# Kernel optimization log

Measured on AMD Instinct MI355X. Metric: run time of the kernel, lower is better.

Reference implementation:

```python
import jax, jax.numpy as jnp
import numpy as np

DECAY = 0.9  # decay_const buffer (learn_decay=False)


def setup_inputs() -> dict:
    key = jax.random.key(0)
    ks = jax.random.split(key, 6)
    B, T, D = 64, 512, 768
    spk_hist = jax.random.normal(ks[0], (B, T, D), dtype=jnp.float32)
    act_hist = jax.random.normal(ks[1], (B, T, D), dtype=jnp.float32)
    spk_mask = jax.random.randint(ks[2], (B, T), 0, 2).astype(jnp.float32)
    act_mask = jax.random.randint(ks[3], (B, T), 0, 2).astype(jnp.float32)
    spk_mean = jax.random.normal(ks[4], (B, D), dtype=jnp.float32)
    act_mean = jax.random.normal(ks[5], (B, D), dtype=jnp.float32)
    mix_logits = jnp.zeros((2,), dtype=jnp.float32)
    return {"spk_hist": spk_hist, "spk_mask": spk_mask,
            "act_hist": act_hist, "act_mask": act_mask,
            "spk_mean": spk_mean, "act_mean": act_mean,
            "mix_logits": mix_logits}


def ema_pool(X, mask, decay):
    # X: [B,T,D], mask: [B,T] (1 valid, 0 pad) -> (h [B,D], has_any [B])
    B, T, D = X.shape
    one_minus = 1.0 - decay

    def step(carry, xm):
        h, has_any = carry          # [B,D], [B,1]
        xt, mt = xm                 # [B,D], [B]
        mt = mt[:, None]            # [B,1]
        h_new = decay * h + one_minus * xt
        h = mt * h_new + (1.0 - mt) * h
        has_any = jnp.minimum(has_any + mt, 1.0)
        return (h, has_any), None

    h0 = jnp.zeros((B, D), X.dtype)
    a0 = jnp.zeros((B, 1), X.dtype)
    (h, has_any), _ = jax.lax.scan(
        step, (h0, a0), (jnp.swapaxes(X, 0, 1), mask.T))
    return h, has_any[:, 0]


def reference(spk_hist, spk_mask, act_hist, act_mask, spk_mean, act_mean, mix_logits):
    c_spk, spk_nonempty = ema_pool(spk_hist, spk_mask, DECAY)
    c_act, act_nonempty = ema_pool(act_hist, act_mask, DECAY)
    c_spk = jnp.where((spk_nonempty == 0)[:, None], spk_mean, c_spk)
    c_act = jnp.where((act_nonempty == 0)[:, None], act_mean, c_act)
    w = jax.nn.softmax(mix_logits, axis=0)
    c = w[0] * c_spk + w[1] * c_act
    return (c, c_spk, c_act, w)
```

## Files before the change

kernel.cpp:

```cpp
#include <hip/hip_runtime.h>

#define B 64
#define T 512
#define D 768
#define NSEG 8
#define TSEG 64
#define LOG2_DECAY (-0.15200309344504995f)

#define WS_P  0
#define WS_NE (2 * B * NSEG * D)

__global__ __launch_bounds__(192) void pool_kernel(
    const float* __restrict__ spk_hist, const float* __restrict__ act_hist,
    const float* __restrict__ spk_mask, const float* __restrict__ act_mask,
    float* __restrict__ ws)
{
    const int blk = blockIdx.x;
    const int seg = blk & (NSEG - 1);
    const int b   = (blk >> 3) & (B - 1);
    const int s   = blk >> 9;

    const int tid  = threadIdx.x;
    const int lane = tid & 63;
    const int wave = tid >> 6;

    __shared__ float    wsm[TSEG];
    __shared__ float    cw[TSEG];
    __shared__ int      ct[TSEG];
    __shared__ unsigned wt[2];
    __shared__ int      Mcnt;

    const float* mask = s ? act_mask : spk_mask;
    unsigned bits = 0, cnt = 0;
    if (tid < 128) {
        const float4 mv = ((const float4*)(mask + b * T))[tid];
        bits = (mv.x > 0.5f ? 1u : 0u) | (mv.y > 0.5f ? 2u : 0u) |
               (mv.z > 0.5f ? 4u : 0u) | (mv.w > 0.5f ? 8u : 0u);
        cnt = __popc(bits);
    }
    unsigned v = cnt;
    #pragma unroll
    for (int off = 1; off < 64; off <<= 1) {
        const unsigned u = __shfl_up(v, off);
        if (lane >= off) v += u;
    }
    if (wave < 2 && lane == 63) wt[wave] = v;
    __syncthreads();
    const unsigned S = wt[0] + wt[1];

    if (tid >= seg * 16 && tid < (seg + 1) * 16) {
        unsigned run = (v - cnt) + (wave == 1 ? wt[0] : 0u);
        const int lbase = (tid - seg * 16) * 4;
        #pragma unroll
        for (int j = 0; j < 4; ++j) {
            float w = 0.0f;
            if (bits & (1u << j)) {
                run += 1;
                w = 0.1f * exp2f((float)(S - run) * LOG2_DECAY);
            }
            wsm[lbase + j] = w;
        }
    }
    __syncthreads();

    if (tid < 64) {
        const float wv = wsm[tid];
        const unsigned long long bal = __ballot(wv != 0.0f);
        if (wv != 0.0f) {
            const int pos = __popcll(bal & ((1ull << tid) - 1ull));
            cw[pos] = wv;
            ct[pos] = tid;
        }
        if (tid == 0) Mcnt = __popcll(bal);
    }
    __syncthreads();

    const float* hist = s ? act_hist : spk_hist;
    const float* Xb = hist + (size_t)(b * T + seg * TSEG) * D + tid * 4;

    float4 acc = make_float4(0.f, 0.f, 0.f, 0.f);
    const int M = Mcnt;
    int k = 0;
    for (; k + 4 <= M; k += 4) {
        const int   t0 = ct[k],   t1 = ct[k+1], t2 = ct[k+2], t3 = ct[k+3];
        const float w0 = cw[k],   w1 = cw[k+1], w2 = cw[k+2], w3 = cw[k+3];
        const float4 x0 = *(const float4*)(Xb + t0 * D);
        const float4 x1 = *(const float4*)(Xb + t1 * D);
        const float4 x2 = *(const float4*)(Xb + t2 * D);
        const float4 x3 = *(const float4*)(Xb + t3 * D);
        acc.x = fmaf(w0, x0.x, acc.x); acc.y = fmaf(w0, x0.y, acc.y);
        acc.z = fmaf(w0, x0.z, acc.z); acc.w = fmaf(w0, x0.w, acc.w);
        acc.x = fmaf(w1, x1.x, acc.x); acc.y = fmaf(w1, x1.y, acc.y);
        acc.z = fmaf(w1, x1.z, acc.z); acc.w = fmaf(w1, x1.w, acc.w);
        acc.x = fmaf(w2, x2.x, acc.x); acc.y = fmaf(w2, x2.y, acc.y);
        acc.z = fmaf(w2, x2.z, acc.z); acc.w = fmaf(w2, x2.w, acc.w);
        acc.x = fmaf(w3, x3.x, acc.x); acc.y = fmaf(w3, x3.y, acc.y);
        acc.z = fmaf(w3, x3.z, acc.z); acc.w = fmaf(w3, x3.w, acc.w);
    }
    for (; k < M; ++k) {
        const float w = cw[k];
        const float4 x = *(const float4*)(Xb + ct[k] * D);
        acc.x = fmaf(w, x.x, acc.x); acc.y = fmaf(w, x.y, acc.y);
        acc.z = fmaf(w, x.z, acc.z); acc.w = fmaf(w, x.w, acc.w);
    }

    *(float4*)(ws + WS_P + ((size_t)((s * B + b) * NSEG + seg)) * D + tid * 4) = acc;
    if (tid == 0 && seg == 0)
        ws[WS_NE + s * B + b] = (S > 0) ? 1.0f : 0.0f;
}

__global__ __launch_bounds__(256) void epilogue_kernel(
    const float* __restrict__ spk_mean, const float* __restrict__ act_mean,
    const float* __restrict__ logits, const float* __restrict__ ws,
    float* __restrict__ out)
{
    const int i4 = blockIdx.x * 256 + threadIdx.x;
    if (i4 >= B * D / 4) return;
    const int b   = i4 / (D / 4);
    const int idx = i4 * 4;
    const int dd  = idx - b * D;

    float4 hs = make_float4(0.f, 0.f, 0.f, 0.f);
    float4 ha = make_float4(0.f, 0.f, 0.f, 0.f);
    #pragma unroll
    for (int seg = 0; seg < NSEG; ++seg) {
        const float4 ps = *(const float4*)(ws + WS_P + (size_t)((0 * B + b) * NSEG + seg) * D + dd);
        const float4 pa = *(const float4*)(ws + WS_P + (size_t)((1 * B + b) * NSEG + seg) * D + dd);
        hs.x += ps.x; hs.y += ps.y; hs.z += ps.z; hs.w += ps.w;
        ha.x += pa.x; ha.y += pa.y; ha.z += pa.z; ha.w += pa.w;
    }

    const float l0 = logits[0], l1 = logits[1];
    const float mx = fmaxf(l0, l1);
    const float e0 = __expf(l0 - mx), e1 = __expf(l1 - mx);
    const float inv = 1.0f / (e0 + e1);
    const float w0 = e0 * inv, w1 = e1 * inv;

    const bool nes = ws[WS_NE + b]     > 0.0f;
    const bool nea = ws[WS_NE + B + b] > 0.0f;
    const float4 cs = nes ? hs : *(const float4*)(spk_mean + idx);
    const float4 ca = nea ? ha : *(const float4*)(act_mean + idx);

    float4 c;
    c.x = w0 * cs.x + w1 * ca.x;
    c.y = w0 * cs.y + w1 * ca.y;
    c.z = w0 * cs.z + w1 * ca.z;
    c.w = w0 * cs.w + w1 * ca.w;

    *(float4*)(out + idx)             = c;
    *(float4*)(out + B * D + idx)     = cs;
    *(float4*)(out + 2 * B * D + idx) = ca;
    if (i4 == 0) {
        out[3 * B * D]     = w0;
        out[3 * B * D + 1] = w1;
    }
}

extern "C" void kernel_launch(void* const* d_in, const int* in_sizes, int n_in,
                              void* d_out, int out_size, void* d_ws, size_t ws_size,
                              hipStream_t stream) {
    const float* spk_hist = (const float*)d_in[0];
    const float* spk_mask = (const float*)d_in[1];
    const float* act_hist = (const float*)d_in[2];
    const float* act_mask = (const float*)d_in[3];
    const float* spk_mean = (const float*)d_in[4];
    const float* act_mean = (const float*)d_in[5];
    const float* logits   = (const float*)d_in[6];
    float* ws  = (float*)d_ws;
    float* out = (float*)d_out;

    pool_kernel<<<2 * B * NSEG, 192, 0, stream>>>(spk_hist, act_hist, spk_mask, act_mask, ws);
    epilogue_kernel<<<(B * D / 4 + 255) / 256, 256, 0, stream>>>(spk_mean, act_mean, logits, ws, out);
}
```

Measured before the change: 207.9 us.

## Truncate EMA to last 128 valid steps and split work evenly across segments

Builds a compacted list of only the most recent 128 valid timesteps per batch row, since older terms carry geometrically negligible weight (decay^128). Each of the 8 segment blocks then processes an equal chunk of that list instead of a fixed time window. This roughly halves the history rows read from memory and balances load across blocks. It trades exactness for a tiny truncation error and drops one shared-memory compaction pass.

Result: faster. 193.8 us (-6.8%).

```diff
diff --git a/kernel.cpp b/kernel.cpp
--- a/kernel.cpp
+++ b/kernel.cpp
@@ -4,7 +4,7 @@
 #define T 512
 #define D 768
 #define NSEG 8
-#define TSEG 64
+#define KMAX 128
 #define LOG2_DECAY (-0.15200309344504995f)
 
 #define WS_P  0
@@ -24,11 +24,9 @@
     const int lane = tid & 63;
     const int wave = tid >> 6;
 
-    __shared__ float    wsm[TSEG];
-    __shared__ float    cw[TSEG];
-    __shared__ int      ct[TSEG];
+    __shared__ float    cw[KMAX];
+    __shared__ int      ct[KMAX];
     __shared__ unsigned wt[2];
-    __shared__ int      Mcnt;
 
     const float* mask = s ? act_mask : spk_mask;
     unsigned bits = 0, cnt = 0;
@@ -46,42 +44,37 @@
     }
     if (wave < 2 && lane == 63) wt[wave] = v;
     __syncthreads();
-    const unsigned S = wt[0] + wt[1];
 
-    if (tid >= seg * 16 && tid < (seg + 1) * 16) {
-        unsigned run = (v - cnt) + (wave == 1 ? wt[0] : 0u);
-        const int lbase = (tid - seg * 16) * 4;
+    const int S    = (int)(wt[0] + wt[1]);
+    const int Kq   = (S < KMAX) ? S : KMAX;
+    const int drop = S - Kq;
+
+    if (tid < 128 && bits) {
+        int run = (int)(v - cnt) + (wave == 1 ? (int)wt[0] : 0);
         #pragma unroll
         for (int j = 0; j < 4; ++j) {
-            float w = 0.0f;
             if (bits & (1u << j)) {
-                run += 1;
-                w = 0.1f * exp2f((float)(S - run) * LOG2_DECAY);
+                ++run;
+                if (run > drop) {
+                    const int pos = run - drop - 1;
+                    cw[pos] = 0.1f * exp2f((float)(S - run) * LOG2_DECAY);
+                    ct[pos] = tid * 4 + j;
+                }
             }
-            wsm[lbase + j] = w;
         }
     }
     __syncthreads();
 
-    if (tid < 64) {
-        const float wv = wsm[tid];
-        const unsigned long long bal = __ballot(wv != 0.0f);
-        if (wv != 0.0f) {
-            const int pos = __popcll(bal & ((1ull << tid) - 1ull));
-            cw[pos] = wv;
-            ct[pos] = tid;
-        }
-        if (tid == 0) Mcnt = __popcll(bal);
-    }
-    __syncthreads();
+    const int chunk = (Kq + NSEG - 1) >> 3;
+    const int k0 = seg * chunk;
+    const int k1 = (k0 + chunk < Kq) ? (k0 + chunk) : Kq;
 
     const float* hist = s ? act_hist : spk_hist;
-    const float* Xb = hist + (size_t)(b * T + seg * TSEG) * D + tid * 4;
+    const float* Xb = hist + (size_t)b * T * D + tid * 4;
 
     float4 acc = make_float4(0.f, 0.f, 0.f, 0.f);
-    const int M = Mcnt;
-    int k = 0;
-    for (; k + 4 <= M; k += 4) {
+    int k = k0;
+    for (; k + 4 <= k1; k += 4) {
         const int   t0 = ct[k],   t1 = ct[k+1], t2 = ct[k+2], t3 = ct[k+3];
         const float w0 = cw[k],   w1 = cw[k+1], w2 = cw[k+2], w3 = cw[k+3];
         const float4 x0 = *(const float4*)(Xb + t0 * D);
@@ -97,7 +90,7 @@
         acc.x = fmaf(w3, x3.x, acc.x); acc.y = fmaf(w3, x3.y, acc.y);
         acc.z = fmaf(w3, x3.z, acc.z); acc.w = fmaf(w3, x3.w, acc.w);
     }
-    for (; k < M; ++k) {
+    for (; k < k1; ++k) {
         const float w = cw[k];
         const float4 x = *(const float4*)(Xb + ct[k] * D);
         acc.x = fmaf(w, x.x, acc.x); acc.y = fmaf(w, x.y, acc.y);
```
